# Kernel optimization log

Measured on AMD Instinct MI355X. Metric: run time of the kernel, lower is better.

## Reference

```python
import jax, jax.numpy as jnp
import numpy as np

N_QUBITS = 16
N_LAYERS = 3
N_CLASSES = 3
PI = 3.14159265  # matches literal in the cudaq kernel


def _apply_1q(state, U, axis):
    # state: (2,)*n complex; U: (2,2). Contract gate into qubit `axis`.
    s = jnp.moveaxis(state, axis, 0)
    s = jnp.tensordot(U, s, axes=1)
    return jnp.moveaxis(s, 0, axis)


def _cnot(state, c, t):
    # slice control axis; X (flip) on target where control==1
    s0 = jax.lax.index_in_dim(state, 0, axis=c, keepdims=False)
    s1 = jax.lax.index_in_dim(state, 1, axis=c, keepdims=False)
    tt = t - (1 if t > c else 0)  # target axis index after removing control axis
    s1 = jnp.flip(s1, axis=tt)
    return jnp.stack([s0, s1], axis=c)


def _simulate(data, params):
    n, L = N_QUBITS, N_LAYERS
    state = jnp.zeros((2 ** n,), jnp.complex64).at[0].set(1.0).reshape((2,) * n)
    for layer in range(L):
        base = layer * 2 * n
        # data re-uploading Ry(data[i]*pi + theta)
        for i in range(n):
            th = 0.5 * (data[i] * PI + params[base + i])
            c, s = jnp.cos(th), jnp.sin(th)
            U = jnp.stack([jnp.stack([c, -s]), jnp.stack([s, c])]).astype(jnp.complex64)
            state = _apply_1q(state, U, i)
        # ring CNOT entanglement
        for i in range(n - 1):
            state = _cnot(state, i, i + 1)
        state = _cnot(state, n - 1, 0)
        # trainable Rz (diagonal -> elementwise multiply)
        for i in range(n):
            phi = 0.5 * params[base + n + i]
            d = jnp.stack([jnp.exp(-1j * phi), jnp.exp(1j * phi)]).astype(jnp.complex64)
            shp = [1] * n
            shp[i] = 2
            state = state * d.reshape(shp)
    probs = jnp.abs(state) ** 2  # real float32
    exps = []
    for q in range(N_CLASSES):  # <Z_q> = P(q=0) - P(q=1)
        p = jnp.moveaxis(probs, q, 0).reshape(2, -1).sum(axis=1)
        exps.append(p[0] - p[1])
    return jnp.stack(exps)


def setup_inputs() -> dict:
    key = jax.random.key(0)
    kx, kp = jax.random.split(key)
    x = jax.random.normal(kx, (512, N_QUBITS), dtype=jnp.float32)
    params = jax.random.normal(kp, (N_LAYERS * 2 * N_QUBITS,), dtype=jnp.float32) * 0.1
    return {"x": x, "params": params}


def reference(x, params):
    # batched statevector simulation; logits: (B, N_CLASSES) float32
    return jax.vmap(_simulate, in_axes=(0, None))(x, params)
```

## Files before the change

### kernel.cpp

```cpp
#include <hip/hip_runtime.h>
#include <hip/hip_bf16.h>
#include <hip/hip_fp16.h>

#define PI_F 3.14159265f


__device__ __forceinline__ unsigned swz(unsigned l){ return l ^ ((l>>5)&31u); }

__device__ __forceinline__ float2 cmul(float2 a, float2 b){
    return make_float2(a.x*b.x - a.y*b.y, a.x*b.y + a.y*b.x);
}

__device__ __forceinline__ void ry_pair(float2& A0, float2& A1, float c, float s){
    float2 a0=A0, a1=A1;
    A0 = make_float2(c*a0.x - s*a1.x, c*a0.y - s*a1.y);
    A1 = make_float2(s*a0.x + c*a1.x, s*a0.y + c*a1.y);
}

__device__ __forceinline__ __half2 h2swap(__half2 v){
    unsigned u = *reinterpret_cast<unsigned*>(&v);
    u = (u>>16) | (u<<16);
    return *reinterpret_cast<__half2*>(&u);
}
__device__ __forceinline__ void ry_h(__half2& A0, __half2& A1,
                                     __half2 c2, __half2 s2, __half2 ns2){
    __half2 n0 = __hfma2(ns2, A1, __hmul2(c2, A0));
    __half2 n1 = __hfma2(s2,  A0, __hmul2(c2, A1));
    A0 = n0; A1 = n1;
}
__device__ __forceinline__ __half2 crot_h(__half2 v, __half2 wxx, __half2 wyn){
    return __hfma2(v, wxx, __hmul2(h2swap(v), wyn));
}

#define RYH(BIT, F) { const __half2 c2=__float2half2_rn(c##F), s2=__float2half2_rn(s##F), ns2=__hneg2(s2); \
    _Pragma("unroll") for (int j=0;j<16;j++){ if (j&(BIT)) continue; ry_h(h[j],h[j|(BIT)],c2,s2,ns2);} }

__global__ __launch_bounds__(512, 4) void k_all(const float* __restrict__ xg,
                                                const float* __restrict__ pg,
                                                __half2* __restrict__ st)
{
    __shared__ __half2 tile[8192];
    __shared__ float cA[16], sA[16], cB[16], sB[16], cC[16], sC[16], phz1[16], phz2[16];
    __shared__ float2 K4[4], D1[16];
    __shared__ __half2 E2Ax[16], E2Ay[16], E2Bx[8], E2By[8],
                       E2Cx[8], E2Cy[8], E2Dx[8], E2Dy[8];
    const int tid = threadIdx.x;
    const int b = blockIdx.x >> 3;
    const unsigned outer = blockIdx.x & 7u;

    if (tid < 16){
        int j = tid, q = 15 - j;
        float th = 0.5f*(xg[b*16+q]*PI_F + pg[q]);
        __sincosf(th, &sA[j], &cA[j]);
    } else if (tid < 32){
        int j = tid-16, q = 15 - j;
        float th = 0.5f*(xg[b*16+q]*PI_F + pg[32+q]);
        __sincosf(th, &sB[j], &cB[j]);
    } else if (tid < 48){
        int j = tid-32, q = 15 - j;
        float th = 0.5f*(xg[b*16+q]*PI_F + pg[64+q]);
        __sincosf(th, &sC[j], &cC[j]);
    } else if (tid < 64){
        int j = tid-48, q = 15 - j;
        phz1[j] = 0.5f*pg[16+q];
    } else if (tid < 80){
        int j = tid-64, q = 15 - j;
        phz2[j] = 0.5f*pg[48+q];
    }
    __syncthreads();
    if (tid < 4){
        const unsigned o13=outer&1u, o14=(outer>>1)&1u, o15=(outer>>2)&1u;
        const unsigned h13=o13^o14, h14=o14^o15, h15=o15;
        const int f0b=(tid>>1)&1, f12b=tid&1;
        float Kr=0.f, Ki=0.f;
        #pragma unroll
        for (int g=0; g<8; ++g){
            const unsigned g13=g&1u, g14=(g>>1)&1u, g15=(g>>2)&1u;
            float w;
            w  = (h13==g13)? cB[13] : (h13? sB[13] : -sB[13]);
            w *= (h14==g14)? cB[14] : (h14? sB[14] : -sB[14]);
            w *= (h15==g15)? cB[15] : (h15? sB[15] : -sB[15]);
            w *= (f12b^(int)g13)?          sA[12]:cA[12];
            w *= ((int)(g13^g14))?         sA[13]:cA[13];
            w *= ((int)g14^f0b^(int)g15)?  sA[14]:cA[14];
            w *= (f0b^(int)g15)?           sA[15]:cA[15];
            float phg = (g13? phz1[13]:-phz1[13]) + (g14? phz1[14]:-phz1[14])
                      + (g15? phz1[15]:-phz1[15]);
            float sn,cs; __sincosf(phg,&sn,&cs);
            Kr += w*cs; Ki += w*sn;
        }
        K4[tid] = make_float2(Kr,Ki);
    } else if (tid>=16 && tid<32){
        const int ii = tid-16;
        float d=0.f;
        #pragma unroll
        for (int j=0;j<4;j++) d += ((ii>>j)&1)? phz1[9+j]:-phz1[9+j];
        float sn,cs; __sincosf(d,&sn,&cs); D1[ii]=make_float2(cs,sn);
    } else if (tid>=32 && tid<48){
        const int ii = tid-32;
        float d=0.f;
        #pragma unroll
        for (int j=0;j<4;j++) d += ((ii>>j)&1)? phz2[9+j]:-phz2[9+j];
        float sn,cs; __sincosf(d,&sn,&cs);
        E2Ax[ii]=__float2half2_rn(cs);
        E2Ay[ii]=__halves2half2(__float2half(-sn), __float2half(sn));
    } else if (tid>=48 && tid<56){
        const int ii = tid-48;
        float d=0.f;
        #pragma unroll
        for (int j=0;j<3;j++) d += ((ii>>j)&1)? phz2[6+j]:-phz2[6+j];
        float sn,cs; __sincosf(d,&sn,&cs);
        E2Bx[ii]=__float2half2_rn(cs);
        E2By[ii]=__halves2half2(__float2half(-sn), __float2half(sn));
    } else if (tid>=56 && tid<64){
        const int ii = tid-56;
        float d=0.f;
        #pragma unroll
        for (int j=0;j<3;j++) d += ((ii>>j)&1)? phz2[3+j]:-phz2[3+j];
        float sn,cs; __sincosf(d,&sn,&cs);
        E2Cx[ii]=__float2half2_rn(cs);
        E2Cy[ii]=__halves2half2(__float2half(-sn), __float2half(sn));
    } else if (tid>=64 && tid<72){
        const int ii = tid-64;
        float d=0.f;
        #pragma unroll
        for (int j=0;j<3;j++) d += ((ii>>j)&1)? phz2[j]:-phz2[j];
        d += (outer&1u)?      phz2[13]:-phz2[13];
        d += ((outer>>1)&1u)? phz2[14]:-phz2[14];
        float sn,cs; __sincosf(d,&sn,&cs);
        E2Dx[ii]=__float2half2_rn(cs);
        E2Dy[ii]=__halves2half2(__float2half(-sn), __float2half(sn));
    }
    __syncthreads();

    const unsigned t = tid;
    __half2 h[16];
    {
        float base_t = 1.0f;
        #pragma unroll
        for (int j=0;j<8;j++){
            int v = (int)(((t>>j)^(t>>(j+1)))&1u);
            base_t *= v? sA[j]:cA[j];
        }
        float pht = 0.f;
        #pragma unroll
        for (int j=0;j<9;j++) pht += ((t>>j)&1u)? phz1[j]:-phz1[j];
        float Ety,Etx; __sincosf(pht,&Ety,&Etx);
        const float2 Et = make_float2(Etx,Ety);
        const unsigned t0 = t&1u;
        const float2 EK0 = cmul(Et, K4[t0<<1]);
        const float2 EK1 = cmul(Et, K4[(t0<<1)|1u]);
        const int t8 = (int)((t>>8)&1u);
        #pragma unroll
        for (int i=0;i<16;i++){
            const int i0=i&1, i1=(i>>1)&1, i2=(i>>2)&1, i3=(i>>3)&1;
            float pr = base_t;
            pr *= (t8^i0)? sA[8] :cA[8];
            pr *= (i0^i1)? sA[9] :cA[9];
            pr *= (i1^i2)? sA[10]:cA[10];
            pr *= (i2^i3)? sA[11]:cA[11];
            float2 w = cmul(D1[i], i3? EK1:EK0);
            h[i] = __float22half2_rn(make_float2(pr*w.x, pr*w.y));
        }
    }
    { const float cF=cB[9],  sF=sB[9];  RYH(1, F) }
    { const float cF=cB[10], sF=sB[10]; RYH(2, F) }
    { const float cF=cB[11], sF=sB[11]; RYH(4, F) }
    { const float cF=cB[12], sF=sB[12]; RYH(8, F) }
    if (outer & 1u){
        #pragma unroll
        for (int j=0;j<16;j++){ if (j&8) continue; __half2 tm=h[j]; h[j]=h[j|8]; h[j|8]=tm; }
    }
    #pragma unroll
    for (int j=0;j<16;j++){ if (j&4) continue; if ((j>>3)&1){ __half2 tm=h[j]; h[j]=h[j|4]; h[j|4]=tm; } }
    #pragma unroll
    for (int j=0;j<16;j++){ if (j&2) continue; if ((j>>2)&1){ __half2 tm=h[j]; h[j]=h[j|2]; h[j|2]=tm; } }
    #pragma unroll
    for (int j=0;j<16;j++){ if (j&1) continue; if ((j>>1)&1){ __half2 tm=h[j]; h[j]=h[j|1]; h[j|1]=tm; } }
    #pragma unroll
    for (int i=0;i<16;i++) h[i] = crot_h(h[i], E2Ax[i], E2Ay[i]);
    { const float cF=cC[10], sF=sC[10]; RYH(2, F) }
    { const float cF=cC[11], sF=sC[11]; RYH(4, F) }
    { const float cF=cC[12], sF=sC[12]; RYH(8, F) }
    #pragma unroll
    for (int i=0;i<16;i++) tile[swz(t | ((unsigned)i<<9))] = h[i];
    __syncthreads();
    #pragma unroll
    for (int i=0;i<16;i++) h[i] = tile[swz((t&63u) | ((unsigned)i<<6) | ((t>>6)<<10))];
    { const float cF=cB[6], sF=sB[6]; RYH(1, F) }
    { const float cF=cB[7], sF=sB[7]; RYH(2, F) }
    { const float cF=cB[8], sF=sB[8]; RYH(4, F) }
    #pragma unroll
    for (int j=0;j<16;j++){ if (j&4) continue; if ((j>>3)&1){ __half2 tm=h[j]; h[j]=h[j|4]; h[j|4]=tm; } }
    #pragma unroll
    for (int j=0;j<16;j++){ if (j&2) continue; if ((j>>2)&1){ __half2 tm=h[j]; h[j]=h[j|2]; h[j|2]=tm; } }
    #pragma unroll
    for (int j=0;j<16;j++){ if (j&1) continue; if ((j>>1)&1){ __half2 tm=h[j]; h[j]=h[j|1]; h[j|1]=tm; } }
    #pragma unroll
    for (int i=0;i<16;i++) h[i] = crot_h(h[i], E2Bx[i&7], E2By[i&7]);
    { const float cF=cC[7], sF=sC[7]; RYH(2, F) }
    { const float cF=cC[8], sF=sC[8]; RYH(4, F) }
    { const float cF=cC[9], sF=sC[9]; RYH(8, F) }
    #pragma unroll
    for (int i=0;i<16;i++) tile[swz((t&63u) | ((unsigned)i<<6) | ((t>>6)<<10))] = h[i];
    __syncthreads();
    #pragma unroll
    for (int i=0;i<16;i++) h[i] = tile[swz((t&7u) | ((unsigned)i<<3) | ((t>>3)<<7))];
    { const float cF=cB[3], sF=sB[3]; RYH(1, F) }
    { const float cF=cB[4], sF=sB[4]; RYH(2, F) }
    { const float cF=cB[5], sF=sB[5]; RYH(4, F) }
    #pragma unroll
    for (int j=0;j<16;j++){ if (j&4) continue; if ((j>>3)&1){ __half2 tm=h[j]; h[j]=h[j|4]; h[j|4]=tm; } }
    #pragma unroll
    for (int j=0;j<16;j++){ if (j&2) continue; if ((j>>2)&1){ __half2 tm=h[j]; h[j]=h[j|2]; h[j|2]=tm; } }
    #pragma unroll
    for (int j=0;j<16;j++){ if (j&1) continue; if ((j>>1)&1){ __half2 tm=h[j]; h[j]=h[j|1]; h[j|1]=tm; } }
    #pragma unroll
    for (int i=0;i<16;i++) h[i] = crot_h(h[i], E2Cx[i&7], E2Cy[i&7]);
    { const float cF=cC[4], sF=sC[4]; RYH(2, F) }
    { const float cF=cC[5], sF=sC[5]; RYH(4, F) }
    { const float cF=cC[6], sF=sC[6]; RYH(8, F) }
    #pragma unroll
    for (int i=0;i<16;i++) tile[swz((t&7u) | ((unsigned)i<<3) | ((t>>3)<<7))] = h[i];
    __syncthreads();
    #pragma unroll
    for (int i=0;i<16;i++) h[i] = tile[swz((unsigned)i | (t<<4))];
    { const float cF=cB[0], sF=sB[0]; RYH(1, F) }
    { const float cF=cB[1], sF=sB[1]; RYH(2, F) }
    { const float cF=cB[2], sF=sB[2]; RYH(4, F) }
    #pragma unroll
    for (int j=0;j<16;j++){ if (j&4) continue; if ((j>>3)&1){ __half2 tm=h[j]; h[j]=h[j|4]; h[j|4]=tm; } }
    #pragma unroll
    for (int j=0;j<16;j++){ if (j&2) continue; if ((j>>2)&1){ __half2 tm=h[j]; h[j]=h[j|2]; h[j|2]=tm; } }
    #pragma unroll
    for (int j=0;j<16;j++){ if (j&1) continue; if ((j>>1)&1){ __half2 tm=h[j]; h[j]=h[j|1]; h[j|1]=tm; } }
    #pragma unroll
    for (int i=0;i<16;i++) h[i] = crot_h(h[i], E2Dx[i&7], E2Dy[i&7]);
    { const float cF=cC[1], sF=sC[1]; RYH(2, F) }
    { const float cF=cC[2], sF=sC[2]; RYH(4, F) }
    { const float cF=cC[3], sF=sC[3]; RYH(8, F) }
    __syncthreads();
    #pragma unroll
    for (int i=0;i<16;i++) tile[swz((unsigned)i | (t<<4))] = h[i];
    __syncthreads();
    __half2* hp = st + ((size_t)b<<16);
    #pragma unroll
    for (int u=0;u<4;u++){
        __half2 hv[4];
        #pragma unroll
        for (int k=0;k<4;k++)
            hv[k] = tile[swz((unsigned)k | (t<<2) | ((unsigned)u<<11))];
        *reinterpret_cast<uint4*>(hp + ((t<<2) | ((unsigned)u<<11) | (outer<<13))) =
            *reinterpret_cast<uint4*>(hv);
    }
}

__global__ __launch_bounds__(256) void k_fin(const float* __restrict__ xg,
                                             const float* __restrict__ pg,
                                             const __half2* __restrict__ st,
                                             float* __restrict__ outg)
{
    __shared__ float cN[16], sN[16];
    __shared__ float snp, csp;
    __shared__ float red[4][3];
    const int tid = threadIdx.x;
    const int b = blockIdx.x >> 3;
    const unsigned outer = blockIdx.x & 7u;
    if (tid < 16){
        int j=tid, q=15-j;
        float th = 0.5f*(xg[b*16+q]*PI_F + pg[64 + q]);
        float s,c; __sincosf(th,&s,&c);
        cN[j]=c; sN[j]=s;
    }
    if (tid==16){ float phi = 0.5f*pg[48 + 0]; float s,c; __sincosf(phi,&s,&c); snp=s; csp=c; }
    __syncthreads();
    const unsigned t = tid;
    const __half2* sp = st + ((size_t)b<<16);
    float2 a[32];
    #pragma unroll
    for (int u=0;u<8;u++){
        unsigned fb = (t<<2) | (outer<<10) | ((unsigned)u<<13);
        uint4 raw = *reinterpret_cast<const uint4*>(sp + fb);
        const __half2* hv = reinterpret_cast<const __half2*>(&raw);
        a[4*u+0] = __half22float2(hv[0]);
        a[4*u+1] = __half22float2(hv[1]);
        a[4*u+2] = __half22float2(hv[2]);
        a[4*u+3] = __half22float2(hv[3]);
    }
    #pragma unroll
    for (int j=0;j<32;j++){ if (j&16) continue; if (j&1){ float2 tm=a[j]; a[j]=a[j|16]; a[j|16]=tm; } }
    #pragma unroll
    for (int j=0;j<32;j++){
        float sn = ((j>>4)&1)? snp : -snp;
        float2 v=a[j];
        a[j]=make_float2(v.x*csp - v.y*sn, v.x*sn + v.y*csp);
    }
    #pragma unroll
    for (int j=0;j<32;j++){ if (j&1)  continue; ry_pair(a[j],a[j|1] ,cN[0] ,sN[0]);  }
    #pragma unroll
    for (int j=0;j<32;j++){ if (j&4)  continue; ry_pair(a[j],a[j|4] ,cN[13],sN[13]); }
    #pragma unroll
    for (int j=0;j<32;j++){ if (j&8)  continue; ry_pair(a[j],a[j|8] ,cN[14],sN[14]); }
    #pragma unroll
    for (int j=0;j<32;j++){ if (j&16) continue; ry_pair(a[j],a[j|16],cN[15],sN[15]); }
    const int pto = (__popc(t) + __popc(outer)) & 1;
    float v0=0.f, v1=0.f, v2=0.f;
    #pragma unroll
    for (int i=0;i<32;i++){
        const int i0=i&1, i1=(i>>1)&1, i2=(i>>2)&1, i3=(i>>3)&1, i4=(i>>4)&1;
        const float pr = a[i].x*a[i].x + a[i].y*a[i].y;
        v0 += (i0^i1^i2^i3^pto)? -pr : pr;
        v1 += (i3^i4)?           -pr : pr;
        v2 += (i2^i3^i4)?        -pr : pr;
    }
    #pragma unroll
    for (int off=32; off>0; off>>=1){
        v0 += __shfl_down(v0, off);
        v1 += __shfl_down(v1, off);
        v2 += __shfl_down(v2, off);
    }
    const int wv = tid>>6, ln = tid&63;
    if (ln==0){ red[wv][0]=v0; red[wv][1]=v1; red[wv][2]=v2; }
    __syncthreads();
    if (tid<3){
        float s = red[0][tid]+red[1][tid]+red[2][tid]+red[3][tid];
        atomicAdd(&outg[b*3+tid], s);
    }
}

extern "C" void kernel_launch(void* const* d_in, const int* in_sizes, int n_in,
                              void* d_out, int out_size, void* d_ws, size_t ws_size,
                              hipStream_t stream)
{
    const float* x = (const float*)d_in[0];
    const float* params = (const float*)d_in[1];
    float* out = (float*)d_out;
    __half2* st = (__half2*)d_ws;
    const int B = in_sizes[0] / 16;

    hipMemsetAsync(d_out, 0, (size_t)out_size*sizeof(float), stream);

    const size_t per = (size_t)65536 * sizeof(__half2);
    int chunk = (int)(ws_size / per);
    if (chunk > 512) chunk = 512;
    if (chunk < 1) chunk = 1;
    if (chunk > B) chunk = B;
    for (int b0=0; b0<B; b0+=chunk){
        const int nb = (B-b0 < chunk) ? (B-b0) : chunk;
        const float* xb = x + (size_t)b0*16;
        float* ob = out + (size_t)b0*3;
        hipLaunchKernelGGL(k_all, dim3(nb*8), dim3(512), 0, stream, xb, params, st);
        hipLaunchKernelGGL(k_fin, dim3(nb*8), dim3(256), 0, stream, xb, params, st, ob);
    }
}
```

Before: 139.7 us.

## Precompute per-thread initial-state factors in shared table and use half2 gates in final kernel

The first kernel now precomputes a 64-entry shared table V that folds the Ry products for qubits 8-11, the phase D1 and the K4 factors. Each thread then builds its 16 initial amplitudes with one complex multiply per entry instead of repeated selects and products. This adds one extra __syncthreads. The final kernel keeps amplitudes in packed half2 and applies the Rz and Ry gates with half2 FMA instead of converting to float2 first. That lowers register use and ALU work but adds fp16 rounding error to the last gates.

```diff
diff --git a/kernel.cpp b/kernel.cpp
--- a/kernel.cpp
+++ b/kernel.cpp
@@ -9,12 +9,6 @@
 
 __device__ __forceinline__ float2 cmul(float2 a, float2 b){
     return make_float2(a.x*b.x - a.y*b.y, a.x*b.y + a.y*b.x);
-}
-
-__device__ __forceinline__ void ry_pair(float2& A0, float2& A1, float c, float s){
-    float2 a0=A0, a1=A1;
-    A0 = make_float2(c*a0.x - s*a1.x, c*a0.y - s*a1.y);
-    A1 = make_float2(s*a0.x + c*a1.x, s*a0.y + c*a1.y);
 }
 
 __device__ __forceinline__ __half2 h2swap(__half2 v){
@@ -34,6 +28,8 @@
 
 #define RYH(BIT, F) { const __half2 c2=__float2half2_rn(c##F), s2=__float2half2_rn(s##F), ns2=__hneg2(s2); \
     _Pragma("unroll") for (int j=0;j<16;j++){ if (j&(BIT)) continue; ry_h(h[j],h[j|(BIT)],c2,s2,ns2);} }
+#define RYH32(BIT, CC, SS) { const __half2 c2=__float2half2_rn(CC), s2=__float2half2_rn(SS), ns2=__hneg2(s2); \
+    _Pragma("unroll") for (int j=0;j<32;j++){ if (j&(BIT)) continue; ry_h(h[j],h[j|(BIT)],c2,s2,ns2);} }
 
 __global__ __launch_bounds__(512, 4) void k_all(const float* __restrict__ xg,
                                                 const float* __restrict__ pg,
@@ -41,7 +37,7 @@
 {
     __shared__ __half2 tile[8192];
     __shared__ float cA[16], sA[16], cB[16], sB[16], cC[16], sC[16], phz1[16], phz2[16];
-    __shared__ float2 K4[4], D1[16];
+    __shared__ float2 K4[4], V[64];
     __shared__ __half2 E2Ax[16], E2Ay[16], E2Bx[8], E2By[8],
                        E2Cx[8], E2Cy[8], E2Dx[8], E2Dy[8];
     const int tid = threadIdx.x;
@@ -90,12 +86,6 @@
             Kr += w*cs; Ki += w*sn;
         }
         K4[tid] = make_float2(Kr,Ki);
-    } else if (tid>=16 && tid<32){
-        const int ii = tid-16;
-        float d=0.f;
-        #pragma unroll
-        for (int j=0;j<4;j++) d += ((ii>>j)&1)? phz1[9+j]:-phz1[9+j];
-        float sn,cs; __sincosf(d,&sn,&cs); D1[ii]=make_float2(cs,sn);
     } else if (tid>=32 && tid<48){
         const int ii = tid-32;
         float d=0.f;
@@ -132,6 +122,22 @@
         E2Dy[ii]=__halves2half2(__float2half(-sn), __float2half(sn));
     }
     __syncthreads();
+    if (tid < 64){
+        const int i  = tid & 15;
+        const int t0b = (tid>>4)&1, t8b = (tid>>5)&1;
+        const int i0=i&1, i1=(i>>1)&1, i2=(i>>2)&1, i3=(i>>3)&1;
+        float G = ((t8b^i0)? sA[8] :cA[8])
+                * ((i0^i1)?  sA[9] :cA[9])
+                * ((i1^i2)?  sA[10]:cA[10])
+                * ((i2^i3)?  sA[11]:cA[11]);
+        float d = 0.f;
+        #pragma unroll
+        for (int j=0;j<4;j++) d += ((i>>j)&1)? phz1[9+j]:-phz1[9+j];
+        float sn,cs; __sincosf(d,&sn,&cs);
+        float2 K = K4[(t0b<<1)|i3];
+        V[tid] = make_float2(G*(cs*K.x - sn*K.y), G*(cs*K.y + sn*K.x));
+    }
+    __syncthreads();
 
     const unsigned t = tid;
     __half2 h[16];
@@ -145,22 +151,13 @@
         float pht = 0.f;
         #pragma unroll
         for (int j=0;j<9;j++) pht += ((t>>j)&1u)? phz1[j]:-phz1[j];
-        float Ety,Etx; __sincosf(pht,&Ety,&Etx);
-        const float2 Et = make_float2(Etx,Ety);
-        const unsigned t0 = t&1u;
-        const float2 EK0 = cmul(Et, K4[t0<<1]);
-        const float2 EK1 = cmul(Et, K4[(t0<<1)|1u]);
-        const int t8 = (int)((t>>8)&1u);
+        float Ey,Ex; __sincosf(pht,&Ey,&Ex);
+        Ex *= base_t; Ey *= base_t;
+        const float2* Vb = V + ((((t>>8)&1u)<<5) | ((t&1u)<<4));
         #pragma unroll
         for (int i=0;i<16;i++){
-            const int i0=i&1, i1=(i>>1)&1, i2=(i>>2)&1, i3=(i>>3)&1;
-            float pr = base_t;
-            pr *= (t8^i0)? sA[8] :cA[8];
-            pr *= (i0^i1)? sA[9] :cA[9];
-            pr *= (i1^i2)? sA[10]:cA[10];
-            pr *= (i2^i3)? sA[11]:cA[11];
-            float2 w = cmul(D1[i], i3? EK1:EK0);
-            h[i] = __float22half2_rn(make_float2(pr*w.x, pr*w.y));
+            const float2 v = Vb[i];
+            h[i] = __float22half2_rn(make_float2(Ex*v.x - Ey*v.y, Ex*v.y + Ey*v.x));
         }
     }
     { const float cF=cB[9],  sF=sB[9];  RYH(1, F) }
@@ -276,39 +273,34 @@
     __syncthreads();
     const unsigned t = tid;
     const __half2* sp = st + ((size_t)b<<16);
-    float2 a[32];
+    __half2 h[32];
     #pragma unroll
     for (int u=0;u<8;u++){
         unsigned fb = (t<<2) | (outer<<10) | ((unsigned)u<<13);
         uint4 raw = *reinterpret_cast<const uint4*>(sp + fb);
         const __half2* hv = reinterpret_cast<const __half2*>(&raw);
-        a[4*u+0] = __half22float2(hv[0]);
-        a[4*u+1] = __half22float2(hv[1]);
-        a[4*u+2] = __half22float2(hv[2]);
-        a[4*u+3] = __half22float2(hv[3]);
-    }
-    #pragma unroll
-    for (int j=0;j<32;j++){ if (j&16) continue; if (j&1){ float2 tm=a[j]; a[j]=a[j|16]; a[j|16]=tm; } }
-    #pragma unroll
-    for (int j=0;j<32;j++){
-        float sn = ((j>>4)&1)? snp : -snp;
-        float2 v=a[j];
-        a[j]=make_float2(v.x*csp - v.y*sn, v.x*sn + v.y*csp);
-    }
-    #pragma unroll
-    for (int j=0;j<32;j++){ if (j&1)  continue; ry_pair(a[j],a[j|1] ,cN[0] ,sN[0]);  }
-    #pragma unroll
-    for (int j=0;j<32;j++){ if (j&4)  continue; ry_pair(a[j],a[j|4] ,cN[13],sN[13]); }
-    #pragma unroll
-    for (int j=0;j<32;j++){ if (j&8)  continue; ry_pair(a[j],a[j|8] ,cN[14],sN[14]); }
-    #pragma unroll
-    for (int j=0;j<32;j++){ if (j&16) continue; ry_pair(a[j],a[j|16],cN[15],sN[15]); }
+        h[4*u+0]=hv[0]; h[4*u+1]=hv[1]; h[4*u+2]=hv[2]; h[4*u+3]=hv[3];
+    }
+    #pragma unroll
+    for (int j=0;j<32;j++){ if (j&16) continue; if (j&1){ __half2 tm=h[j]; h[j]=h[j|16]; h[j|16]=tm; } }
+    {
+        const __half2 wxx = __float2half2_rn(csp);
+        const __half2 wyp = __halves2half2(__float2half(-snp), __float2half(snp));
+        const __half2 wym = __halves2half2(__float2half( snp), __float2half(-snp));
+        #pragma unroll
+        for (int j=0;j<32;j++) h[j] = crot_h(h[j], wxx, (j&16)? wyp : wym);
+    }
+    RYH32(1,  cN[0],  sN[0])
+    RYH32(4,  cN[13], sN[13])
+    RYH32(8,  cN[14], sN[14])
+    RYH32(16, cN[15], sN[15])
     const int pto = (__popc(t) + __popc(outer)) & 1;
     float v0=0.f, v1=0.f, v2=0.f;
     #pragma unroll
     for (int i=0;i<32;i++){
         const int i0=i&1, i1=(i>>1)&1, i2=(i>>2)&1, i3=(i>>3)&1, i4=(i>>4)&1;
-        const float pr = a[i].x*a[i].x + a[i].y*a[i].y;
+        const float2 a = __half22float2(h[i]);
+        const float pr = a.x*a.x + a.y*a.y;
         v0 += (i0^i1^i2^i3^pto)? -pr : pr;
         v1 += (i3^i4)?           -pr : pr;
         v2 += (i2^i3^i4)?        -pr : pr;
```

Measured after the change: 132.1 us. 1.06x faster.
